# Performance work log

Measured on AMD Instinct MI355X. Metric: run time of the kernel, lower is better.

Reference implementation:

```python
import jax, jax.numpy as jnp
import numpy as np

HEADS, DH, HID, EDGE_D = 8, 16, 128, 32  # heads, head_dim, hidden_dim, edge_dim
N, E = 50000, 800000


def _ln(x, w, b):
    mu = jnp.mean(x, axis=-1, keepdims=True)
    var = jnp.var(x, axis=-1, keepdims=True)
    return (x - mu) * jax.lax.rsqrt(var + 1e-5) * w + b


def setup_inputs() -> dict:
    key = jax.random.key(0)
    ks = jax.random.split(key, 16)
    lin = lambda k, fi, fo: (jax.random.normal(k, (fi, fo), jnp.float32) / np.sqrt(fi).astype(np.float32))
    inp = {
        'x': jax.random.normal(ks[0], (N, HID), jnp.float32),
        'edge_index': jax.random.randint(ks[1], (2, E), 0, N, jnp.int32),
        'edge_attr': jax.random.normal(ks[2], (E, EDGE_D), jnp.float32),
        'Wq': lin(ks[3], HID, HID), 'bq': jnp.zeros((HID,), jnp.float32),
        'Wk': lin(ks[4], HID, HID), 'bk': jnp.zeros((HID,), jnp.float32),
        'Wv': lin(ks[5], HID, HID), 'bv': jnp.zeros((HID,), jnp.float32),
        'We': lin(ks[6], EDGE_D, HID), 'be': jnp.zeros((HID,), jnp.float32),
        'Wskip': lin(ks[7], HID, HID), 'bskip': jnp.zeros((HID,), jnp.float32),
        'ln1_w': jnp.ones((HID,), jnp.float32), 'ln1_b': jnp.zeros((HID,), jnp.float32),
        'W1': lin(ks[8], HID, 4 * HID), 'b1': jnp.zeros((4 * HID,), jnp.float32),
        'W2': lin(ks[9], 4 * HID, HID), 'b2': jnp.zeros((HID,), jnp.float32),
        'ln2_w': jnp.ones((HID,), jnp.float32), 'ln2_b': jnp.zeros((HID,), jnp.float32),
    }
    return inp


def reference(x, edge_index, edge_attr, Wq, bq, Wk, bk, Wv, bv, We, be,
              Wskip, bskip, ln1_w, ln1_b, W1, b1, W2, b2, ln2_w, ln2_b):
    n = x.shape[0]
    src, dst = edge_index[0], edge_index[1]

    h = _ln(x, ln1_w, ln1_b)
    # projections, then per-edge gathers -> [E, H, Dh]
    q = (h @ Wq + bq)[dst].reshape(-1, HEADS, DH)
    k = (h @ Wk + bk)[src].reshape(-1, HEADS, DH)
    v = (h @ Wv + bv)[src].reshape(-1, HEADS, DH)
    e = (edge_attr @ We + be).reshape(-1, HEADS, DH)
    k = k + e
    v = v + e

    alpha = jnp.einsum('ehd,ehd->eh', q, k) / np.sqrt(DH).astype(np.float32)  # [E, H]
    # segment softmax over destination nodes (PyG softmax semantics)
    amax = jax.ops.segment_max(alpha, dst, num_segments=n)
    amax = jnp.where(jnp.isfinite(amax), amax, 0.0)
    expa = jnp.exp(alpha - amax[dst])
    denom = jax.ops.segment_sum(expa, dst, num_segments=n)
    alpha = expa / (denom[dst] + 1e-16)

    msg = jax.ops.segment_sum(alpha[..., None] * v, dst, num_segments=n)  # [N, H, Dh]
    conv_out = msg.reshape(n, HID) + h @ Wskip + bskip  # root_weight skip

    x = x + conv_out
    h2 = _ln(x, ln2_w, ln2_b)
    ffn = jax.nn.gelu(h2 @ W1 + b1, approximate=False) @ W2 + b2
    return x + ffn
```

## Files before the change

### kernel.cpp

```cpp
#include <hip/hip_runtime.h>
#include <math.h>

#define HID 128
#define EDGE_D 32
#define SC 0.36067376f

typedef unsigned short u16;
typedef unsigned int u32;
typedef __bf16 bf16x8 __attribute__((ext_vector_type(8)));
typedef float f32x4 __attribute__((ext_vector_type(4)));
typedef u32 u32x4 __attribute__((ext_vector_type(4)));
typedef u32 u32x2 __attribute__((ext_vector_type(2)));

static __device__ __forceinline__ u16 f2bf(float f) {
  u32 u = __float_as_uint(f);
  u += 0x7fffu + ((u >> 16) & 1u);
  return (u16)(u >> 16);
}
static __device__ __forceinline__ u32 pack2(float a, float b) {
  return (u32)f2bf(a) | ((u32)f2bf(b) << 16);
}
static __device__ __forceinline__ float bflo(u32 w) { return __uint_as_float(w << 16); }
static __device__ __forceinline__ float bfhi(u32 w) { return __uint_as_float(w & 0xffff0000u); }
static __device__ __forceinline__ float grp16_sum(float x) {
  x += __int_as_float(__builtin_amdgcn_mov_dpp(__float_as_int(x), 0x128, 0xf, 0xf, true));
  x += __int_as_float(__builtin_amdgcn_mov_dpp(__float_as_int(x), 0x124, 0xf, 0xf, true));
  x += __int_as_float(__builtin_amdgcn_mov_dpp(__float_as_int(x), 0x122, 0xf, 0xf, true));
  x += __int_as_float(__builtin_amdgcn_mov_dpp(__float_as_int(x), 0x121, 0xf, 0xf, true));
  return x;
}
static __device__ __forceinline__ float wave_allreduce_sum(float v) {
#pragma unroll
  for (int off = 32; off > 0; off >>= 1) v += __shfl_xor(v, off);
  return v;
}

__global__ __launch_bounds__(256) void ln_kernel(const float* __restrict__ in,
                                                 u16* __restrict__ out,
                                                 const float* __restrict__ w,
                                                 const float* __restrict__ b, int n) {
  int row0 = blockIdx.x * 4 + (threadIdx.x >> 6);
  int lane = threadIdx.x & 63;
  int stride = gridDim.x * 4;
  for (int row = row0; row < n; row += stride) {
    const float* p = in + (size_t)row * HID;
    float a = p[lane], c = p[lane + 64];
    float s = wave_allreduce_sum(a + c);
    float s2 = wave_allreduce_sum(a * a + c * c);
    float mean = s * (1.f / 128.f);
    float var = s2 * (1.f / 128.f) - mean * mean;
    float rs = rsqrtf(var + 1e-5f);
    u16* o = out + (size_t)row * HID;
    o[lane] = f2bf((a - mean) * rs * w[lane] + b[lane]);
    o[lane + 64] = f2bf((c - mean) * rs * w[lane + 64] + b[lane + 64]);
  }
}

__global__ __launch_bounds__(256) void convert_weights(
    const float* __restrict__ Wq, const float* __restrict__ Wk,
    const float* __restrict__ Wv, const float* __restrict__ Ws,
    const float* __restrict__ W1, const float* __restrict__ W2,
    const float* __restrict__ We, u16* __restrict__ WqkvsT,
    u16* __restrict__ W1T, u16* __restrict__ W2T, u16* __restrict__ WbdT,
    int* __restrict__ cnt, int Nn) {
  int idx = blockIdx.x * 256 + threadIdx.x;
  if (idx < 65536) {
    int m = idx >> 7, k = idx & 127;
    const float* Wm = m < 128 ? Wq : m < 256 ? Wk : m < 384 ? Wv : Ws;
    WqkvsT[idx] = f2bf(Wm[k * 128 + (m & 127)]);
  } else if (idx < 131072) {
    int j = idx - 65536;
    int m = j >> 7, k = j & 127;
    W1T[j] = f2bf(W1[k * 512 + m]);
  } else if (idx < 196608) {
    int j = idx - 131072;
    int m = j >> 9, k = j & 511;
    W2T[j] = f2bf(W2[k * 128 + m]);
  } else if (idx < 229376) {
    int j = idx - 196608;
    int m = j >> 8, c = j & 255;
    WbdT[j] = ((c >> 5) == (m >> 4)) ? f2bf(We[(c & 31) * 128 + m]) : (u16)0;
  } else if (idx < 229376 + Nn) {
    cnt[idx - 229376] = 0;
  }
}

#define GSTAGE(buf, kc)                                                        \
  {                                                                            \
    _Pragma("unroll") for (int i = 0; i < 2; i++) {                            \
      int idx = i * 256 + t;                                                   \
      int row = idx >> 2, c4 = idx & 3;                                        \
      __builtin_amdgcn_global_load_lds(                                        \
          (const __attribute__((address_space(1))) u32*)(A + (size_t)(r0 + row) * K + (kc) + c4 * 8), \
          (__attribute__((address_space(3))) u32*)&As[buf][idx * 8], 16, 0, 0);\
      __builtin_amdgcn_global_load_lds(                                        \
          (const __attribute__((address_space(1))) u32*)(Bt + (size_t)(c0 + row) * K + (kc) + c4 * 8), \
          (__attribute__((address_space(3))) u32*)&Bs[buf][idx * 8], 16, 0, 0);\
    }                                                                          \
  }

#define GEMM_CORE                                                              \
  constexpr int NT = K / 32;                                                   \
  GSTAGE(0, 0)                                                                 \
  __syncthreads();                                                             \
  _Pragma("unroll") for (int tt = 0; tt < NT; tt++) {                          \
    if (tt + 1 < NT) GSTAGE((tt + 1) & 1, (tt + 1) * 32)                       \
    bf16x8 a0 = *(const bf16x8*)&As[tt & 1][(w * 32 + sr) * 32 + g * 8];       \
    bf16x8 a1 = *(const bf16x8*)&As[tt & 1][(w * 32 + 16 + sr) * 32 + g * 8];  \
    _Pragma("unroll") for (int nn = 0; nn < 8; nn++) {                         \
      bf16x8 b = *(const bf16x8*)&Bs[tt & 1][(nn * 16 + sr) * 32 + g * 8];     \
      acc[0][nn] = __builtin_amdgcn_mfma_f32_16x16x32_bf16(a0, b, acc[0][nn], 0, 0, 0); \
      acc[1][nn] = __builtin_amdgcn_mfma_f32_16x16x32_bf16(a1, b, acc[1][nn], 0, 0, 0); \
    }                                                                          \
    __syncthreads();                                                           \
  }

template <int EPI, int K>
__global__ __launch_bounds__(256) void gemm_bf16(
    const u16* __restrict__ A, const u16* __restrict__ Bt, int n,
    const float* __restrict__ bias0, const float* __restrict__ bias1,
    const float* __restrict__ bias2,
    float* __restrict__ of0, u32* __restrict__ opq, u32* __restrict__ pkv,
    u16* __restrict__ ob1, const float* __restrict__ addsrc) {
  __shared__ u16 As[2][128 * 32];
  __shared__ u16 Bs[2][128 * 32];
  int t = threadIdx.x;
  int w = t >> 6, lane = t & 63;
  int g = lane >> 4, sr = lane & 15;
  int r0 = blockIdx.x * 128;
  int c0 = blockIdx.y * 128;
  f32x4 acc[2][8];
#pragma unroll
  for (int m = 0; m < 2; m++)
#pragma unroll
    for (int nn = 0; nn < 8; nn++) acc[m][nn] = {0.f, 0.f, 0.f, 0.f};

  GEMM_CORE

  if (EPI == 0 && blockIdx.y == 0) {
#pragma unroll
    for (int m = 0; m < 2; m++)
#pragma unroll
      for (int nn = 0; nn < 4; nn++)
#pragma unroll
        for (int j = 0; j < 4; j++) {
          int row = r0 + w * 32 + m * 16 + g * 4 + j;
          if (row < n) {
            int cj = nn * 16 + sr;
            opq[((size_t)row << 6) + cj] =
                pack2(acc[m][nn][j] + bias0[cj], acc[m][nn + 4][j] + bias0[cj + 64]);
          }
        }
    return;
  }
  if (EPI == 0) {
    const float* bp = blockIdx.y == 1 ? bias1 : bias2;
    int which = blockIdx.y - 1;
#pragma unroll
    for (int m = 0; m < 2; m++)
#pragma unroll
      for (int nn = 0; nn < 4; nn++)
#pragma unroll
        for (int j = 0; j < 4; j++) {
          int row = r0 + w * 32 + m * 16 + g * 4 + j;
          if (row < n) {
            int cj = nn * 16 + sr;
            pkv[((size_t)row << 7) + (cj << 1) + which] =
                pack2(acc[m][nn][j] + bp[cj], acc[m][nn + 4][j] + bp[cj + 64]);
          }
        }
    return;
  }
#pragma unroll
  for (int m = 0; m < 2; m++)
#pragma unroll
    for (int nn = 0; nn < 8; nn++)
#pragma unroll
      for (int j = 0; j < 4; j++) {
        int row = r0 + w * 32 + m * 16 + g * 4 + j;
        if (row < n) {
          int cj = nn * 16 + sr;
          float val = acc[m][nn][j];
          if (EPI == 1) {
            int cjg = blockIdx.y * 128 + cj;
            float v2 = val + bias0[cjg];
            v2 = 0.5f * v2 * (1.f + erff(v2 * 0.70710678118f));
            ob1[(size_t)row * 512 + cjg] = f2bf(v2);
          } else {
            of0[(size_t)row * HID + cj] = val + bias0[cj] + addsrc[(size_t)row * HID + cj];
          }
        }
      }
}

__global__ __launch_bounds__(256) void gemm_bd_fin(
    const u16* __restrict__ Aw, const u16* __restrict__ BtW,
    const u16* __restrict__ Ah, const u16* __restrict__ BtS, int n,
    const float* __restrict__ x, const float* __restrict__ msg,
    const float* __restrict__ be, const float* __restrict__ bskip,
    const float* __restrict__ lnw, const float* __restrict__ lnb,
    float* __restrict__ x1, u16* __restrict__ h2) {
  __shared__ u16 As[2][128 * 32];
  __shared__ u16 Bs[2][128 * 32];
  int t = threadIdx.x;
  int w = t >> 6, lane = t & 63;
  int g = lane >> 4, sr = lane & 15;
  int r0 = blockIdx.x * 128;
  int c0 = 0;
  f32x4 acc[2][8];
#pragma unroll
  for (int m = 0; m < 2; m++)
#pragma unroll
    for (int nn = 0; nn < 8; nn++) acc[m][nn] = {0.f, 0.f, 0.f, 0.f};

  {
    const u16* A = Aw;
    const u16* Bt = BtW;
    constexpr int K = 256;
    GEMM_CORE
  }
  {
    const u16* A = Ah;
    const u16* Bt = BtS;
    constexpr int K = 128;
    GEMM_CORE
  }

  float becol[8], wcol[8], bcol[8], bscol[8];
#pragma unroll
  for (int nn = 0; nn < 8; nn++) {
    int c = nn * 16 + sr;
    becol[nn] = be[c];
    bscol[nn] = bskip[c];
    wcol[nn] = lnw[c];
    bcol[nn] = lnb[c];
  }
#pragma unroll
  for (int m = 0; m < 2; m++)
#pragma unroll
    for (int j = 0; j < 4; j++) {
      int row = r0 + w * 32 + m * 16 + g * 4 + j;
      if (row < n) {
        const float* xr = x + (size_t)row * HID;
        const float* mr = msg + (size_t)row * HID;
        float* x1r = x1 + (size_t)row * HID;
        float tv[8];
        float s = 0.f, s2 = 0.f;
#pragma unroll
        for (int nn = 0; nn < 8; nn++) {
          int c = nn * 16 + sr;
          float t1 = xr[c] + mr[c] + acc[m][nn][j] + becol[nn] + bscol[nn];
          tv[nn] = t1;
          s += t1;
          s2 = fmaf(t1, t1, s2);
        }
        s = grp16_sum(s);
        s2 = grp16_sum(s2);
        float mean = s * (1.f / 128.f);
        float var = s2 * (1.f / 128.f) - mean * mean;
        float rs = rsqrtf(var + 1e-5f);
        u16* h2r = h2 + (size_t)row * HID;
#pragma unroll
        for (int nn = 0; nn < 8; nn++) {
          int c = nn * 16 + sr;
          x1r[c] = tv[nn];
          h2r[c] = f2bf((tv[nn] - mean) * rs * wcol[nn] + bcol[nn]);
        }
      }
    }
}

__global__ __launch_bounds__(256) void hist_kernel(const int* __restrict__ dstp,
                                                   int* __restrict__ cnt, int E) {
  int i = blockIdx.x * blockDim.x + threadIdx.x;
  int stride = gridDim.x * blockDim.x;
  for (; i < E; i += stride) atomicAdd(&cnt[dstp[i]], 1);
}

__global__ __launch_bounds__(256) void scan_partial(const int* __restrict__ cnt,
                                                    int* __restrict__ bs, int N) {
  __shared__ int sd[256];
  int idx = blockIdx.x * 256 + threadIdx.x;
  sd[threadIdx.x] = (idx < N) ? cnt[idx] : 0;
  __syncthreads();
  for (int s = 128; s > 0; s >>= 1) {
    if (threadIdx.x < s) sd[threadIdx.x] += sd[threadIdx.x + s];
    __syncthreads();
  }
  if (threadIdx.x == 0) bs[blockIdx.x] = sd[0];
}

__global__ __launch_bounds__(256) void scan_bs(const int* __restrict__ bs,
                                               int* __restrict__ bs2, int nb) {
  __shared__ int sd[256];
  int t = threadIdx.x;
  int v = (t < nb) ? bs[t] : 0;
  sd[t] = v;
  __syncthreads();
  for (int s = 1; s < 256; s <<= 1) {
    int add = (t >= s) ? sd[t - s] : 0;
    __syncthreads();
    sd[t] += add;
    __syncthreads();
  }
  bs2[t] = sd[t] - v;
}

__global__ __launch_bounds__(256) void scan_final(const int* __restrict__ cnt,
                                                  const int* __restrict__ bs2,
                                                  int* __restrict__ offs,
                                                  int* __restrict__ woff, int N) {
  __shared__ int sd[256];
  int t = threadIdx.x;
  int idx = blockIdx.x * 256 + t;
  int v = (idx < N) ? cnt[idx] : 0;
  sd[t] = v;
  __syncthreads();
  for (int s = 1; s < 256; s <<= 1) {
    int add = (t >= s) ? sd[t - s] : 0;
    __syncthreads();
    sd[t] += add;
    __syncthreads();
  }
  if (idx < N) {
    int ex = sd[t] - v + bs2[blockIdx.x];
    offs[idx] = ex;
    woff[idx] = ex;
  }
}

__global__ __launch_bounds__(256) void scatter_kernel(const int* __restrict__ ei,
                                                      int* __restrict__ woff,
                                                      int2* __restrict__ sorted,
                                                      int E) {
  int i = blockIdx.x * blockDim.x + threadIdx.x;
  int stride = gridDim.x * blockDim.x;
  for (; i < E; i += stride) {
    int src = ei[i];
    int dst = ei[E + i];
    int pos = atomicAdd(&woff[dst], 1);
    sorted[pos] = make_int2(src, i);
  }
}

__global__ __launch_bounds__(256) void qwe_kernel(const u32* __restrict__ pq,
                                                  const float* __restrict__ We,
                                                  const float* __restrict__ be,
                                                  u32* __restrict__ qweb,
                                                  float* __restrict__ qbe, int Nn) {
  __shared__ float sWe[32][129];
  __shared__ float sbe[128];
  int t = threadIdx.x;
  for (int i = t; i < 32 * 128; i += 256) sWe[i >> 7][i & 127] = We[i];
  if (t < 128) sbe[t] = be[t];
  __syncthreads();
  int lane = t & 63, w = t >> 6;
  int g = lane >> 4, sr = lane & 15;
  int base = lane & 48;
  int stride = gridDim.x * 4;
  for (int node = blockIdx.x * 4 + w; node < Nn; node += stride) {
    u32 pw = pq[(size_t)node * 64 + lane];
    float q0 = bflo(pw), q1 = bfhi(pw);
    float o00 = 0.f, o01 = 0.f, o10 = 0.f, o11 = 0.f;
#pragma unroll
    for (int d0 = 0; d0 < 16; d0++) {
      float qa = __shfl(q0, base + d0);
      float qb = __shfl(q1, base + d0);
      int col = base + d0;
      o00 += qa * sWe[2 * sr][col];
      o01 += qa * sWe[2 * sr + 1][col];
      o10 += qb * sWe[2 * sr][64 + col];
      o11 += qb * sWe[2 * sr + 1][64 + col];
    }
    qweb[(size_t)node * 128 + g * 16 + sr] = pack2(o00 * SC, o01 * SC);
    qweb[(size_t)node * 128 + 64 + g * 16 + sr] = pack2(o10 * SC, o11 * SC);
    float t0 = grp16_sum(q0 * sbe[lane]);
    float t1 = grp16_sum(q1 * sbe[lane + 64]);
    if (sr == 0) {
      qbe[node * 8 + g] = t0 * SC;
      qbe[node * 8 + 4 + g] = t1 * SC;
    }
  }
}

#define ISSUE4(P, base_)                                                       \
  {                                                                            \
    _Pragma("unroll") for (int jj = 0; jj < 4; jj++) {                         \
      int sj = min(base_ + jj, segn - 1);                                      \
      int sxx = __builtin_amdgcn_readlane(seRx, sj);                           \
      int syy = __builtin_amdgcn_readlane(seRy, sj);                           \
      P##kv[jj] = *(const u32x2*)(pkv + ((size_t)sxx << 7) + (lane << 1));     \
      P##ea[jj] = *(const float2*)(eaf + ((size_t)syy << 5) + 2 * sr);         \
    }                                                                          \
  }

#define COMP4(P, base_)                                                        \
  {                                                                            \
    _Pragma("unroll") for (int jj = 0; jj < 4; jj++) {                         \
      u32 kx = P##kv[jj].x, ky = P##kv[jj].y;                                  \
      float ex = P##ea[jj].x, ey = P##ea[jj].y;                                \
      float k0 = bflo(kx), k1 = bfhi(kx);                                      \
      float v0f = bflo(ky), v1f = bfhi(ky);                                    \
      float p0 = fmaf(q0C, k0, fmaf(qw0x, ex, qw0y * ey));                     \
      float p1 = fmaf(q1C, k1, fmaf(qw1x, ex, qw1y * ey));                     \
      p0 = grp16_sum(p0) + qb0C;                                               \
      p1 = grp16_sum(p1) + qb1C;                                               \
      bool val_ = (base_ + jj) < segn;                                         \
      float w1 = val_ ? __builtin_amdgcn_exp2f(p0) : 0.f;                      \
      float w2 = val_ ? __builtin_amdgcn_exp2f(p1) : 0.f;                      \
      l1 += w1;                                                                \
      l2 += w2;                                                                \
      a0 = fmaf(w1, v0f, a0);                                                  \
      a1 = fmaf(w2, v1f, a1);                                                  \
      wa00 = fmaf(w1, ex, wa00);                                               \
      wa01 = fmaf(w1, ey, wa01);                                               \
      wa10 = fmaf(w2, ex, wa10);                                               \
      wa11 = fmaf(w2, ey, wa11);                                               \
    }                                                                          \
  }

__global__ __launch_bounds__(256) void fused_edge(
    const int* __restrict__ offs, const int* __restrict__ cnt,
    const int2* __restrict__ sorted, const float* __restrict__ eaf,
    const float* __restrict__ be, const u32* __restrict__ pq,
    const u32* __restrict__ pkv, const u32* __restrict__ qweb,
    const float* __restrict__ qbe, float* __restrict__ msg,
    u32* __restrict__ weab, int Nn, int Etot) {
  int lane = threadIdx.x & 63;
  int w = threadIdx.x >> 6;
  int g = lane >> 4, sr = lane & 15;
  int wid = blockIdx.x * 4 + w;
  int nw = gridDim.x * 4;
  int per = (Nn + nw - 1) / nw;
  int n0 = wid * per;
  int n1 = min(Nn, n0 + per);
  if (n0 >= n1) return;
  int nn = n1 - n0;

  float be0 = be[lane], be1 = be[lane + 64];

  int ml = min(lane, nn - 1);
  int myBeg = offs[n0 + ml];
  int myCnt = cnt[n0 + ml];

  int beg = __builtin_amdgcn_readlane(myBeg, 0);
  int num = __builtin_amdgcn_readlane(myCnt, 0);
  int2 se2 = sorted[min(beg + min(lane, max(num - 1, 0)), Etot - 1)];
  int seCx = se2.x, seCy = se2.y;
  u32 pqC = pq[(size_t)n0 * 64 + lane];
  u32 qwb0C = qweb[(size_t)n0 * 128 + g * 16 + sr];
  u32 qwb1C = qweb[(size_t)n0 * 128 + 64 + g * 16 + sr];
  float qb0C = qbe[(size_t)n0 * 8 + g], qb1C = qbe[(size_t)n0 * 8 + 4 + g];

  for (int ni = 0; ni < nn; ni++) {
    int node = n0 + ni;
    int begX = 0, numX = 0, seXx = 0, seXy = 0;
    u32 pqX = 0, qwb0X = 0, qwb1X = 0;
    float qb0X = 0.f, qb1X = 0.f;
    if (ni + 1 < nn) {
      begX = __builtin_amdgcn_readlane(myBeg, ni + 1);
      numX = __builtin_amdgcn_readlane(myCnt, ni + 1);
      int2 sx = sorted[min(begX + min(lane, max(numX - 1, 0)), Etot - 1)];
      seXx = sx.x;
      seXy = sx.y;
      pqX = pq[(size_t)(node + 1) * 64 + lane];
      qwb0X = qweb[(size_t)(node + 1) * 128 + g * 16 + sr];
      qwb1X = qweb[(size_t)(node + 1) * 128 + 64 + g * 16 + sr];
      qb0X = qbe[(size_t)(node + 1) * 8 + g];
      qb1X = qbe[(size_t)(node + 1) * 8 + 4 + g];
    }
    float q0C = bflo(pqC) * SC, q1C = bfhi(pqC) * SC;
    float qw0x = bflo(qwb0C), qw0y = bfhi(qwb0C);
    float qw1x = bflo(qwb1C), qw1y = bfhi(qwb1C);
    float l1 = 0.f, l2 = 0.f, a0 = 0.f, a1 = 0.f;
    float wa00 = 0.f, wa01 = 0.f, wa10 = 0.f, wa11 = 0.f;
    if (num > 0) {
      int cb = 0;
      int seRx = seCx, seRy = seCy;
      while (true) {
        int segn = min(num - cb, 64);
        u32x2 Akv[4], Bkv[4];
        float2 Aea[4], Bea[4];
        ISSUE4(A, 0)
        for (int c = 0; c < segn; c += 8) {
          ISSUE4(B, c + 4)
          COMP4(A, c)
          ISSUE4(A, c + 8)
          COMP4(B, c + 4)
        }
        cb += 64;
        if (cb >= num) break;
        int rem = num - cb;
        int2 sn = sorted[min(beg + cb + min(lane, rem - 1), Etot - 1)];
        seRx = sn.x;
        seRy = sn.y;
      }
    }
    float inv1 = 1.f / (l1 + 1e-30f), inv2 = 1.f / (l2 + 1e-30f);
    size_t ob = (size_t)node * HID + lane;
    if (num > 0) {
      msg[ob] = a0 * inv1;
      msg[ob + 64] = a1 * inv2;
    } else {
      msg[ob] = -be0;
      msg[ob + 64] = -be1;
    }
    weab[(size_t)node * 128 + g * 16 + sr] = pack2(wa00 * inv1, wa01 * inv1);
    weab[(size_t)node * 128 + 64 + g * 16 + sr] = pack2(wa10 * inv2, wa11 * inv2);
    beg = begX;
    num = numX;
    seCx = seXx;
    seCy = seXy;
    pqC = pqX;
    qwb0C = qwb0X;
    qwb1C = qwb1X;
    qb0C = qb0X;
    qb1C = qb1X;
  }
}

extern "C" void kernel_launch(void* const* d_in, const int* in_sizes, int n_in,
                              void* d_out, int out_size, void* d_ws, size_t ws_size,
                              hipStream_t stream) {
  const float* x = (const float*)d_in[0];
  const int* ei = (const int*)d_in[1];
  const float* ea = (const float*)d_in[2];
  const float* Wq = (const float*)d_in[3];
  const float* bq = (const float*)d_in[4];
  const float* Wk = (const float*)d_in[5];
  const float* bk = (const float*)d_in[6];
  const float* Wv = (const float*)d_in[7];
  const float* bv = (const float*)d_in[8];
  const float* We = (const float*)d_in[9];
  const float* be = (const float*)d_in[10];
  const float* Wskip = (const float*)d_in[11];
  const float* bskip = (const float*)d_in[12];
  const float* ln1w = (const float*)d_in[13];
  const float* ln1b = (const float*)d_in[14];
  const float* W1 = (const float*)d_in[15];
  const float* b1p = (const float*)d_in[16];
  const float* W2 = (const float*)d_in[17];
  const float* b2p = (const float*)d_in[18];
  const float* ln2w = (const float*)d_in[19];
  const float* ln2b = (const float*)d_in[20];

  int N = in_sizes[0] / HID;
  int E = in_sizes[1] / 2;
  size_t nf = (size_t)N * HID;

  float* ws = (float*)d_ws;
  size_t off = 0;
  u16* h_bf = (u16*)(ws + off); off += nf / 2;
  u32* pq = (u32*)(ws + off); off += nf / 2;
  u32* pkv = (u32*)(ws + off); off += nf;
  float* skipx1 = ws + off; off += nf;
  float* msg = ws + off; off += nf;
  u32* weab = (u32*)(ws + off); off += nf;
  u32* qweb = (u32*)(ws + off); off += nf;
  float* qbe = ws + off; off += (size_t)N * 8;
  int2* sorted = (int2*)(ws + off); off += (size_t)E * 2;
  int* cnt = (int*)(ws + off); off += N;
  int* offs = (int*)(ws + off); off += N;
  int* woff = (int*)(ws + off); off += N;
  int* bs = (int*)(ws + off); off += 256;
  int* bs2 = (int*)(ws + off); off += 256;
  u16* WqkvsT = (u16*)(ws + off); off += 32768;
  u16* W1T = (u16*)(ws + off); off += 32768;
  u16* W2T = (u16*)(ws + off); off += 32768;
  u16* WbdT = (u16*)(ws + off); off += 16384;
  u16* h2o = (u16*)qweb;
  u16* tbf = (u16*)msg;

  convert_weights<<<1092, 256, 0, stream>>>(Wq, Wk, Wv, Wskip, W1, W2, We,
                                            WqkvsT, W1T, W2T, WbdT, cnt, N);

  int ln_blocks = (N + 3) / 4;
  ln_kernel<<<ln_blocks, 256, 0, stream>>>(x, h_bf, ln1w, ln1b, N);

  dim3 gq((N + 127) / 128, 3);
  gemm_bf16<0, 128><<<gq, 256, 0, stream>>>(h_bf, WqkvsT, N, bq, bk, bv,
                                            nullptr, pq, pkv, nullptr, nullptr);

  int nb = (N + 255) / 256;
  hist_kernel<<<1024, 256, 0, stream>>>(ei + E, cnt, E);
  scan_partial<<<nb, 256, 0, stream>>>(cnt, bs, N);
  scan_bs<<<1, 256, 0, stream>>>(bs, bs2, nb);
  scan_final<<<nb, 256, 0, stream>>>(cnt, bs2, offs, woff, N);
  scatter_kernel<<<1024, 256, 0, stream>>>(ei, woff, sorted, E);

  qwe_kernel<<<1024, 256, 0, stream>>>(pq, We, be, qweb, qbe, N);

  int fe_blocks = (N + 15) / 16;
  fused_edge<<<fe_blocks, 256, 0, stream>>>(offs, cnt, sorted, ea, be, pq, pkv,
                                            qweb, qbe, msg, weab, N, E);

  dim3 ge((N + 127) / 128, 1);
  gemm_bd_fin<<<ge, 256, 0, stream>>>((const u16*)weab, WbdT, h_bf,
                                      WqkvsT + 384 * 128, N, x, msg, be, bskip,
                                      ln2w, ln2b, skipx1, h2o);

  dim3 gf1((N + 127) / 128, 4);
  gemm_bf16<1, 128><<<gf1, 256, 0, stream>>>(h2o, W1T, N, b1p, nullptr, nullptr,
                                             nullptr, nullptr, nullptr, tbf, nullptr);
  dim3 gf2((N + 127) / 128, 1);
  gemm_bf16<2, 512><<<gf2, 256, 0, stream>>>(tbf, W2T, N, b2p, nullptr, nullptr,
                                             (float*)d_out, nullptr, nullptr,
                                             nullptr, skipx1);
}
```

Baseline: 429.2 us.

## Fold Wq·We into QKV GEMM, drop qwe kernel, merge scan, bf16 msg

Precomputes a folded weight Wq·We (scaled) and bias on device so the per-node q·We projection is produced as two extra column tiles of the QKV GEMM, removing the separate qwe_kernel. The qbe term is now recomputed in fused_edge from q and be with a group reduction. It also merges the block-scan kernel into scan_final and stores the aggregated messages as bf16 instead of fp32. Together these cut kernel launches and memory traffic, at the cost of a larger GEMM grid, a precomputed bf16 folded weight, and lower message precision.

```diff
diff --git a/kernel.cpp b/kernel.cpp
--- a/kernel.cpp
+++ b/kernel.cpp
@@ -60,8 +60,9 @@
     const float* __restrict__ Wq, const float* __restrict__ Wk,
     const float* __restrict__ Wv, const float* __restrict__ Ws,
     const float* __restrict__ W1, const float* __restrict__ W2,
-    const float* __restrict__ We, u16* __restrict__ WqkvsT,
-    u16* __restrict__ W1T, u16* __restrict__ W2T, u16* __restrict__ WbdT,
+    const float* __restrict__ We, const float* __restrict__ bq,
+    u16* __restrict__ WqkvsT, u16* __restrict__ W1T, u16* __restrict__ W2T,
+    u16* __restrict__ WbdT, u16* __restrict__ WfoldT, float* __restrict__ bfold,
     int* __restrict__ cnt, int Nn) {
   int idx = blockIdx.x * 256 + threadIdx.x;
   if (idx < 65536) {
@@ -80,8 +81,26 @@
     int j = idx - 196608;
     int m = j >> 8, c = j & 255;
     WbdT[j] = ((c >> 5) == (m >> 4)) ? f2bf(We[(c & 31) * 128 + m]) : (u16)0;
-  } else if (idx < 229376 + Nn) {
-    cnt[idx - 229376] = 0;
+  } else if (idx < 262144) {
+    int j = idx - 229376;
+    int m = j >> 7, k = j & 127;
+    int base = (m >> 5) * 16;
+    const float* wq = Wq + k * 128 + base;
+    const float* we = We + (m & 31) * 128 + base;
+    float s = 0.f;
+#pragma unroll
+    for (int t = 0; t < 16; t++) s = fmaf(wq[t], we[t], s);
+    WfoldT[j] = f2bf(s * SC);
+  } else if (idx < 262400) {
+    int m = idx - 262144;
+    int base = (m >> 5) * 16;
+    const float* we = We + (m & 31) * 128 + base;
+    float s = 0.f;
+#pragma unroll
+    for (int t = 0; t < 16; t++) s = fmaf(bq[base + t], we[t], s);
+    bfold[m] = s * SC;
+  } else if (idx < 262400 + Nn) {
+    cnt[idx - 262400] = 0;
   }
 }
 
@@ -117,18 +136,28 @@
 
 template <int EPI, int K>
 __global__ __launch_bounds__(256) void gemm_bf16(
-    const u16* __restrict__ A, const u16* __restrict__ Bt, int n,
+    const u16* __restrict__ A, const u16* __restrict__ BtQ,
+    const u16* __restrict__ BtF, int n,
     const float* __restrict__ bias0, const float* __restrict__ bias1,
-    const float* __restrict__ bias2,
+    const float* __restrict__ bias2, const float* __restrict__ bfold,
     float* __restrict__ of0, u32* __restrict__ opq, u32* __restrict__ pkv,
-    u16* __restrict__ ob1, const float* __restrict__ addsrc) {
+    u16* __restrict__ qweb16, u16* __restrict__ ob1,
+    const float* __restrict__ addsrc) {
   __shared__ u16 As[2][128 * 32];
   __shared__ u16 Bs[2][128 * 32];
   int t = threadIdx.x;
   int w = t >> 6, lane = t & 63;
   int g = lane >> 4, sr = lane & 15;
   int r0 = blockIdx.x * 128;
-  int c0 = blockIdx.y * 128;
+  int c0;
+  const u16* Bt;
+  if (EPI == 0 && blockIdx.y >= 3) {
+    c0 = (blockIdx.y - 3) * 128;
+    Bt = BtF;
+  } else {
+    c0 = blockIdx.y * 128;
+    Bt = BtQ;
+  }
   f32x4 acc[2][8];
 #pragma unroll
   for (int m = 0; m < 2; m++)
@@ -153,7 +182,7 @@
         }
     return;
   }
-  if (EPI == 0) {
+  if (EPI == 0 && blockIdx.y < 3) {
     const float* bp = blockIdx.y == 1 ? bias1 : bias2;
     int which = blockIdx.y - 1;
 #pragma unroll
@@ -167,6 +196,24 @@
             int cj = nn * 16 + sr;
             pkv[((size_t)row << 7) + (cj << 1) + which] =
                 pack2(acc[m][nn][j] + bp[cj], acc[m][nn + 4][j] + bp[cj + 64]);
+          }
+        }
+    return;
+  }
+  if (EPI == 0) {
+    const float* bf = bfold + c0;
+#pragma unroll
+    for (int m = 0; m < 2; m++)
+#pragma unroll
+      for (int nn = 0; nn < 4; nn++)
+#pragma unroll
+        for (int j = 0; j < 4; j++) {
+          int row = r0 + w * 32 + m * 16 + g * 4 + j;
+          if (row < n) {
+            int cj = nn * 16 + sr;
+            u16* qrow = qweb16 + ((size_t)row << 8) + c0;
+            qrow[cj] = f2bf(acc[m][nn][j] + bf[cj]);
+            qrow[cj + 64] = f2bf(acc[m][nn + 4][j] + bf[cj + 64]);
           }
         }
     return;
@@ -196,7 +243,7 @@
 __global__ __launch_bounds__(256) void gemm_bd_fin(
     const u16* __restrict__ Aw, const u16* __restrict__ BtW,
     const u16* __restrict__ Ah, const u16* __restrict__ BtS, int n,
-    const float* __restrict__ x, const float* __restrict__ msg,
+    const float* __restrict__ x, const u32* __restrict__ msgb,
     const float* __restrict__ be, const float* __restrict__ bskip,
     const float* __restrict__ lnw, const float* __restrict__ lnb,
     float* __restrict__ x1, u16* __restrict__ h2) {
@@ -242,14 +289,18 @@
       int row = r0 + w * 32 + m * 16 + g * 4 + j;
       if (row < n) {
         const float* xr = x + (size_t)row * HID;
-        const float* mr = msg + (size_t)row * HID;
+        const u32* mr = msgb + ((size_t)row << 6);
         float* x1r = x1 + (size_t)row * HID;
+        u32 mw[4];
+#pragma unroll
+        for (int nn = 0; nn < 4; nn++) mw[nn] = mr[nn * 16 + sr];
         float tv[8];
         float s = 0.f, s2 = 0.f;
 #pragma unroll
         for (int nn = 0; nn < 8; nn++) {
           int c = nn * 16 + sr;
-          float t1 = xr[c] + mr[c] + acc[m][nn][j] + becol[nn] + bscol[nn];
+          float mval = nn < 4 ? bflo(mw[nn]) : bfhi(mw[nn - 4]);
+          float t1 = xr[c] + mval + acc[m][nn][j] + becol[nn] + bscol[nn];
           tv[nn] = t1;
           s += t1;
           s2 = fmaf(t1, t1, s2);
@@ -290,28 +341,21 @@
   if (threadIdx.x == 0) bs[blockIdx.x] = sd[0];
 }
 
-__global__ __launch_bounds__(256) void scan_bs(const int* __restrict__ bs,
-                                               int* __restrict__ bs2, int nb) {
+__global__ __launch_bounds__(256) void scan_final(const int* __restrict__ cnt,
+                                                  const int* __restrict__ bs,
+                                                  int* __restrict__ offs,
+                                                  int* __restrict__ woff, int N,
+                                                  int nb) {
+  __shared__ int sb[256];
   __shared__ int sd[256];
   int t = threadIdx.x;
-  int v = (t < nb) ? bs[t] : 0;
-  sd[t] = v;
+  sb[t] = (t < nb && t < (int)blockIdx.x) ? bs[t] : 0;
   __syncthreads();
-  for (int s = 1; s < 256; s <<= 1) {
-    int add = (t >= s) ? sd[t - s] : 0;
+  for (int s = 128; s > 0; s >>= 1) {
+    if (t < s) sb[t] += sb[t + s];
     __syncthreads();
-    sd[t] += add;
-    __syncthreads();
-  }
-  bs2[t] = sd[t] - v;
-}
-
-__global__ __launch_bounds__(256) void scan_final(const int* __restrict__ cnt,
-                                                  const int* __restrict__ bs2,
-                                                  int* __restrict__ offs,
-                                                  int* __restrict__ woff, int N) {
-  __shared__ int sd[256];
-  int t = threadIdx.x;
+  }
+  int base = sb[0];
   int idx = blockIdx.x * 256 + t;
   int v = (idx < N) ? cnt[idx] : 0;
   sd[t] = v;
@@ -323,7 +367,7 @@
     __syncthreads();
   }
   if (idx < N) {
-    int ex = sd[t] - v + bs2[blockIdx.x];
+    int ex = sd[t] - v + base;
     offs[idx] = ex;
     woff[idx] = ex;
   }
@@ -340,46 +384,6 @@
     int dst = ei[E + i];
     int pos = atomicAdd(&woff[dst], 1);
     sorted[pos] = make_int2(src, i);
-  }
-}
-
-__global__ __launch_bounds__(256) void qwe_kernel(const u32* __restrict__ pq,
-                                                  const float* __restrict__ We,
-                                                  const float* __restrict__ be,
-                                                  u32* __restrict__ qweb,
-                                                  float* __restrict__ qbe, int Nn) {
-  __shared__ float sWe[32][129];
-  __shared__ float sbe[128];
-  int t = threadIdx.x;
-  for (int i = t; i < 32 * 128; i += 256) sWe[i >> 7][i & 127] = We[i];
-  if (t < 128) sbe[t] = be[t];
-  __syncthreads();
-  int lane = t & 63, w = t >> 6;
-  int g = lane >> 4, sr = lane & 15;
-  int base = lane & 48;
-  int stride = gridDim.x * 4;
-  for (int node = blockIdx.x * 4 + w; node < Nn; node += stride) {
-    u32 pw = pq[(size_t)node * 64 + lane];
-    float q0 = bflo(pw), q1 = bfhi(pw);
-    float o00 = 0.f, o01 = 0.f, o10 = 0.f, o11 = 0.f;
-#pragma unroll
-    for (int d0 = 0; d0 < 16; d0++) {
-      float qa = __shfl(q0, base + d0);
-      float qb = __shfl(q1, base + d0);
-      int col = base + d0;
-      o00 += qa * sWe[2 * sr][col];
-      o01 += qa * sWe[2 * sr + 1][col];
-      o10 += qb * sWe[2 * sr][64 + col];
-      o11 += qb * sWe[2 * sr + 1][64 + col];
-    }
-    qweb[(size_t)node * 128 + g * 16 + sr] = pack2(o00 * SC, o01 * SC);
-    qweb[(size_t)node * 128 + 64 + g * 16 + sr] = pack2(o10 * SC, o11 * SC);
-    float t0 = grp16_sum(q0 * sbe[lane]);
-    float t1 = grp16_sum(q1 * sbe[lane + 64]);
-    if (sr == 0) {
-      qbe[node * 8 + g] = t0 * SC;
-      qbe[node * 8 + 4 + g] = t1 * SC;
-    }
   }
 }
 
@@ -423,9 +427,8 @@
     const int* __restrict__ offs, const int* __restrict__ cnt,
     const int2* __restrict__ sorted, const float* __restrict__ eaf,
     const float* __restrict__ be, const u32* __restrict__ pq,
-    const u32* __restrict__ pkv, const u32* __restrict__ qweb,
-    const float* __restrict__ qbe, float* __restrict__ msg,
-    u32* __restrict__ weab, int Nn, int Etot) {
+    const u32* __restrict__ pkv, const u16* __restrict__ qweb16,
+    u32* __restrict__ msgb, u32* __restrict__ weab, int Nn, int Etot) {
   int lane = threadIdx.x & 63;
   int w = threadIdx.x >> 6;
   int g = lane >> 4, sr = lane & 15;
@@ -448,15 +451,13 @@
   int2 se2 = sorted[min(beg + min(lane, max(num - 1, 0)), Etot - 1)];
   int seCx = se2.x, seCy = se2.y;
   u32 pqC = pq[(size_t)n0 * 64 + lane];
-  u32 qwb0C = qweb[(size_t)n0 * 128 + g * 16 + sr];
-  u32 qwb1C = qweb[(size_t)n0 * 128 + 64 + g * 16 + sr];
-  float qb0C = qbe[(size_t)n0 * 8 + g], qb1C = qbe[(size_t)n0 * 8 + 4 + g];
+  u32 qwb0C = *(const u32*)(qweb16 + ((size_t)n0 << 8) + g * 32 + 2 * sr);
+  u32 qwb1C = *(const u32*)(qweb16 + ((size_t)n0 << 8) + (4 + g) * 32 + 2 * sr);
 
   for (int ni = 0; ni < nn; ni++) {
     int node = n0 + ni;
     int begX = 0, numX = 0, seXx = 0, seXy = 0;
     u32 pqX = 0, qwb0X = 0, qwb1X = 0;
-    float qb0X = 0.f, qb1X = 0.f;
     if (ni + 1 < nn) {
       begX = __builtin_amdgcn_readlane(myBeg, ni + 1);
       numX = __builtin_amdgcn_readlane(myCnt, ni + 1);
@@ -464,14 +465,14 @@
       seXx = sx.x;
       seXy = sx.y;
       pqX = pq[(size_t)(node + 1) * 64 + lane];
-      qwb0X = qweb[(size_t)(node + 1) * 128 + g * 16 + sr];
-      qwb1X = qweb[(size_t)(node + 1) * 128 + 64 + g * 16 + sr];
-      qb0X = qbe[(size_t)(node + 1) * 8 + g];
-      qb1X = qbe[(size_t)(node + 1) * 8 + 4 + g];
+      qwb0X = *(const u32*)(qweb16 + ((size_t)(node + 1) << 8) + g * 32 + 2 * sr);
+      qwb1X = *(const u32*)(qweb16 + ((size_t)(node + 1) << 8) + (4 + g) * 32 + 2 * sr);
     }
     float q0C = bflo(pqC) * SC, q1C = bfhi(pqC) * SC;
     float qw0x = bflo(qwb0C), qw0y = bfhi(qwb0C);
     float qw1x = bflo(qwb1C), qw1y = bfhi(qwb1C);
+    float qb0C = grp16_sum(q0C * be0);
+    float qb1C = grp16_sum(q1C * be1);
     float l1 = 0.f, l2 = 0.f, a0 = 0.f, a1 = 0.f;
     float wa00 = 0.f, wa01 = 0.f, wa10 = 0.f, wa11 = 0.f;
     if (num > 0) {
@@ -497,13 +498,10 @@
       }
     }
     float inv1 = 1.f / (l1 + 1e-30f), inv2 = 1.f / (l2 + 1e-30f);
-    size_t ob = (size_t)node * HID + lane;
     if (num > 0) {
-      msg[ob] = a0 * inv1;
-      msg[ob + 64] = a1 * inv2;
+      msgb[((size_t)node << 6) + lane] = pack2(a0 * inv1, a1 * inv2);
     } else {
-      msg[ob] = -be0;
-      msg[ob + 64] = -be1;
+      msgb[((size_t)node << 6) + lane] = pack2(-be0, -be1);
     }
     weab[(size_t)node * 128 + g * 16 + sr] = pack2(wa00 * inv1, wa01 * inv1);
     weab[(size_t)node * 128 + 64 + g * 16 + sr] = pack2(wa10 * inv2, wa11 * inv2);
@@ -514,8 +512,6 @@
     pqC = pqX;
     qwb0C = qwb0X;
     qwb1C = qwb1X;
-    qb0C = qb0X;
-    qb1C = qb1X;
   }
 }
 
@@ -554,56 +550,57 @@
   u32* pq = (u32*)(ws + off); off += nf / 2;
   u32* pkv = (u32*)(ws + off); off += nf;
   float* skipx1 = ws + off; off += nf;
-  float* msg = ws + off; off += nf;
+  u32* msgb = (u32*)(ws + off); off += nf / 2;
   u32* weab = (u32*)(ws + off); off += nf;
-  u32* qweb = (u32*)(ws + off); off += nf;
-  float* qbe = ws + off; off += (size_t)N * 8;
+  u16* qweb16 = (u16*)(ws + off); off += nf;
   int2* sorted = (int2*)(ws + off); off += (size_t)E * 2;
   int* cnt = (int*)(ws + off); off += N;
   int* offs = (int*)(ws + off); off += N;
   int* woff = (int*)(ws + off); off += N;
   int* bs = (int*)(ws + off); off += 256;
-  int* bs2 = (int*)(ws + off); off += 256;
   u16* WqkvsT = (u16*)(ws + off); off += 32768;
   u16* W1T = (u16*)(ws + off); off += 32768;
   u16* W2T = (u16*)(ws + off); off += 32768;
   u16* WbdT = (u16*)(ws + off); off += 16384;
-  u16* h2o = (u16*)qweb;
-  u16* tbf = (u16*)msg;
-
-  convert_weights<<<1092, 256, 0, stream>>>(Wq, Wk, Wv, Wskip, W1, W2, We,
-                                            WqkvsT, W1T, W2T, WbdT, cnt, N);
+  u16* WfoldT = (u16*)(ws + off); off += 16384;
+  float* bfold = ws + off; off += 256;
+  u16* h2o = (u16*)pq;
+  u16* tbf = (u16*)msgb;
+
+  convert_weights<<<1221, 256, 0, stream>>>(Wq, Wk, Wv, Wskip, W1, W2, We, bq,
+                                            WqkvsT, W1T, W2T, WbdT, WfoldT,
+                                            bfold, cnt, N);
 
   int ln_blocks = (N + 3) / 4;
   ln_kernel<<<ln_blocks, 256, 0, stream>>>(x, h_bf, ln1w, ln1b, N);
 
-  dim3 gq((N + 127) / 128, 3);
-  gemm_bf16<0, 128><<<gq, 256, 0, stream>>>(h_bf, WqkvsT, N, bq, bk, bv,
-                                            nullptr, pq, pkv, nullptr, nullptr);
+  dim3 gq((N + 127) / 128, 5);
+  gemm_bf16<0, 128><<<gq, 256, 0, stream>>>(h_bf, WqkvsT, WfoldT, N, bq, bk, bv,
+                                            bfold, nullptr, pq, pkv, qweb16,
+                                            nullptr, nullptr);
 
   int nb = (N + 255) / 256;
   hist_kernel<<<1024, 256, 0, stream>>>(ei + E, cnt, E);
   scan_partial<<<nb, 256, 0, stream>>>(cnt, bs, N);
-  scan_bs<<<1, 256, 0, stream>>>(bs, bs2, nb);
-  scan_final<<<nb, 256, 0, stream>>>(cnt, bs2, offs, woff, N);
+  scan_final<<<nb, 256, 0, stream>>>(cnt, bs, offs, woff, N, nb);
   scatter_kernel<<<1024, 256, 0, stream>>>(ei, woff, sorted, E);
-
-  qwe_kernel<<<1024, 256, 0, stream>>>(pq, We, be, qweb, qbe, N);
 
   int fe_blocks = (N + 15) / 16;
   fused_edge<<<fe_blocks, 256, 0, stream>>>(offs, cnt, sorted, ea, be, pq, pkv,
-                                            qweb, qbe, msg, weab, N, E);
+                                            qweb16, msgb, weab, N, E);
 
   dim3 ge((N + 127) / 128, 1);
   gemm_bd_fin<<<ge, 256, 0, stream>>>((const u16*)weab, WbdT, h_bf,
-                                      WqkvsT + 384 * 128, N, x, msg, be, bskip,
+                                      WqkvsT + 384 * 128, N, x, msgb, be, bskip,
                                       ln2w, ln2b, skipx1, h2o);
 
   dim3 gf1((N + 127) / 128, 4);
-  gemm_bf16<1, 128><<<gf1, 256, 0, stream>>>(h2o, W1T, N, b1p, nullptr, nullptr,
-                                             nullptr, nullptr, nullptr, tbf, nullptr);
+  gemm_bf16<1, 128><<<gf1, 256, 0, stream>>>(h2o, W1T, nullptr, N, b1p, nullptr,
+                                             nullptr, nullptr, nullptr, nullptr,
+                                             nullptr, nullptr, tbf, nullptr);
   dim3 gf2((N + 127) / 128, 1);
-  gemm_bf16<2, 512><<<gf2, 256, 0, stream>>>(tbf, W2T, N, b2p, nullptr, nullptr,
-                                             (float*)d_out, nullptr, nullptr,
-                                             nullptr, skipx1);
-}
+  gemm_bf16<2, 512><<<gf2, 256, 0, stream>>>(tbf, W2T, nullptr, N, b2p, nullptr,
+                                             nullptr, nullptr, (float*)d_out,
+                                             nullptr, nullptr, nullptr, nullptr,
+                                             skipx1);
+}
```

New measurement: 408.2 us. 1.05x faster.
